# Kernel tuning notes

Hardware: AMD Instinct MI355X
Metric: run time of the kernel (lower is better)

Reference implementation:

```python
import jax, jax.numpy as jnp
import numpy as np

NUM_EMB = 1024
EMB_DIM = 256
COMMITMENT_COST = 0.25


def setup_inputs() -> dict:
    key = jax.random.key(0)
    k1, k2 = jax.random.split(key)
    inp = jax.random.normal(k1, (64, EMB_DIM, 32, 32), dtype=jnp.float32)  # [B, C, H, W]
    emb_weight = jax.random.uniform(
        k2, (NUM_EMB, EMB_DIM), minval=-1.0 / NUM_EMB, maxval=1.0 / NUM_EMB, dtype=jnp.float32
    )
    return {"inp": inp, "emb_weight": emb_weight}


def reference(inp, emb_weight):
    sg = jax.lax.stop_gradient
    x = jnp.transpose(inp, (0, 2, 3, 1))              # [B, H, W, C]
    flat = x.reshape(-1, EMB_DIM)                      # [N, C]
    d = (jnp.sum(flat * flat, axis=1, keepdims=True)
         + jnp.sum(emb_weight * emb_weight, axis=1)
         - 2.0 * (flat @ emb_weight.T))
    idx = jnp.argmin(d, axis=1)                        # [N]
    encodings = jax.nn.one_hot(idx, NUM_EMB, dtype=jnp.float32)  # [N, K]
    e = emb_weight[idx].reshape(x.shape)               # [B, H, W, C]
    loss = jnp.mean((e - sg(x)) ** 2) + COMMITMENT_COST * jnp.mean((sg(e) - x) ** 2)
    e_ste = x + sg(e - x)                              # straight-through estimator
    avg_probs = jnp.mean(encodings, axis=0)
    perplexity = jnp.exp(-jnp.sum(avg_probs * jnp.log(avg_probs + 1e-10)))
    out = jnp.transpose(e_ste, (0, 3, 1, 2))           # back to [B, C, H, W]
    return loss, out, perplexity, encodings
```

## Files before the change

kernel.cpp:

```cpp
#include <hip/hip_runtime.h>
#include <hip/hip_bf16.h>
#include <math.h>
#include <float.h>

#define BB    64
#define CCH   256
#define KKE   1024
#define HWN   1024
#define NTOT  (BB*HWN)
#define OUT_ELE (BB*CCH*HWN)
#define LOSS_OFF 0
#define OUT_OFF  1
#define PERP_OFF (1 + OUT_ELE)
#define ENC_OFF  (2 + OUT_ELE)

#define WS_IDX    0
#define WS_ANORM  262144
#define WS_HIST   524288
#define WS_BNORM  528384
#define WS_MISC   532480
#define WS_LIST   536576
#define WS_EMBT   798720
#define WS_EHI    1847296
#define WS_ELO    2371584
#define WS_CD1    2895872
#define WS_CK1    4993024
#define WS_CD2    7090176

typedef __attribute__((ext_vector_type(4))) float f32x4;
typedef __attribute__((ext_vector_type(8))) short s16x8;

#define TAU 2e-4f

__device__ inline void merge_cand(float& d1, int& k1, float& d2,
                                  float od1, int ok1, float od2) {
    bool w = (od1 < d1) || (od1 == d1 && ok1 < k1);
    float loser_d1 = w ? d1 : od1;
    float winner_d2 = w ? od2 : d2;
    d2 = fminf(winner_d2, loser_d1);
    if (w) { d1 = od1; k1 = ok1; }
}

__global__ __launch_bounds__(256) void prep_kernel(const float* __restrict__ emb,
                                                   float* __restrict__ embT,
                                                   float* __restrict__ bnorm,
                                                   short* __restrict__ ehi,
                                                   short* __restrict__ elo,
                                                   unsigned int* __restrict__ hist,
                                                   float* __restrict__ misc) {
    const int k = blockIdx.x;
    const int t = threadIdx.x;
    float v = emb[k*CCH + t];
    embT[(size_t)t*KKE + k] = v;
    __hip_bfloat16 h = __float2bfloat16(v);
    float hf = __bfloat162float(h);
    __hip_bfloat16 l = __float2bfloat16(v - hf);
    size_t eoff = (size_t)(t >> 5)*32768 + (size_t)k*32 + (t & 31);
    ehi[eoff] = *(short*)&h;
    elo[eoff] = *(short*)&l;
    double sq = (double)v * (double)v;
    #pragma unroll
    for (int off = 32; off; off >>= 1) sq += __shfl_down(sq, off);
    __shared__ double wred[4];
    const int wave = t >> 6, lane = t & 63;
    if (lane == 0) wred[wave] = sq;
    __syncthreads();
    if (t == 0) bnorm[k] = (float)(wred[0] + wred[1] + wred[2] + wred[3]);
    if (blockIdx.x < 4) hist[blockIdx.x*256 + t] = 0u;
    if (blockIdx.x == 4 && t == 0) { misc[0] = 0.0f; ((int*)misc)[1] = 0; }
}

__global__ __launch_bounds__(256) void anorm_kernel(const float* __restrict__ inp,
                                                    float* __restrict__ anorm) {
    const int b  = blockIdx.y;
    const int hw = blockIdx.x * 256 + threadIdx.x;
    const float* p = inp + (size_t)b*CCH*HWN + hw;
    double s = 0.0;
    #pragma unroll 8
    for (int c = 0; c < CCH; ++c) {
        float v = p[(size_t)c*HWN];
        s += (double)v * (double)v;
    }
    anorm[b*HWN + hw] = (float)s;
}

__global__ __launch_bounds__(256, 3) void argmin_mfma(const float* __restrict__ inp,
                                                      const short* __restrict__ ehi,
                                                      const short* __restrict__ elo,
                                                      const float* __restrict__ anorm,
                                                      const float* __restrict__ bnorm,
                                                      float* __restrict__ cd1,
                                                      int* __restrict__ ck1,
                                                      float* __restrict__ cd2) {
    __shared__ short Ahi[128*40];
    __shared__ short Alo[128*40];
    __shared__ short Bhi[128*40];
    __shared__ short Blo[128*40];

    const int t    = threadIdx.x;
    const int w    = t >> 6;
    const int lane = t & 63;
    const int q    = lane >> 4;
    const int l15  = lane & 15;
    const int n0   = blockIdx.x * 128;
    const int k0   = blockIdx.y * 128;
    const int b    = n0 >> 10;
    const int hw0  = n0 & 1023;
    const float* gA = inp + (size_t)b*CCH*HWN + hw0;

    const int na = t & 127;
    const int ch = t >> 7;
    const int br = t >> 2;
    const int bc = (t & 3) * 8;

    f32x4 acc[2][8];
    #pragma unroll
    for (int i = 0; i < 2; ++i)
        #pragma unroll
        for (int j = 0; j < 8; ++j) acc[i][j] = (f32x4){0.f,0.f,0.f,0.f};

    for (int chunk = 0; chunk < 8; ++chunk) {
        const int c0 = chunk * 32;
        __syncthreads();
        float v[16];
        #pragma unroll
        for (int cc = 0; cc < 16; ++cc)
            v[cc] = gA[(size_t)(c0 + ch*16 + cc) * HWN + na];
        short hs[16], ls[16];
        #pragma unroll
        for (int cc = 0; cc < 16; ++cc) {
            __hip_bfloat16 h = __float2bfloat16(v[cc]);
            float hf = __bfloat162float(h);
            __hip_bfloat16 l = __float2bfloat16(v[cc] - hf);
            hs[cc] = *(short*)&h; ls[cc] = *(short*)&l;
        }
        *(s16x8*)&Ahi[na*40 + ch*16]     = *(s16x8*)&hs[0];
        *(s16x8*)&Ahi[na*40 + ch*16 + 8] = *(s16x8*)&hs[8];
        *(s16x8*)&Alo[na*40 + ch*16]     = *(s16x8*)&ls[0];
        *(s16x8*)&Alo[na*40 + ch*16 + 8] = *(s16x8*)&ls[8];
        {
            const size_t ebase = (size_t)chunk*32768 + (size_t)k0*32;
            *(s16x8*)&Bhi[br*40 + bc]        = *(const s16x8*)&ehi[ebase + t*8];
            *(s16x8*)&Bhi[(64+br)*40 + bc]   = *(const s16x8*)&ehi[ebase + 2048 + t*8];
            *(s16x8*)&Blo[br*40 + bc]        = *(const s16x8*)&elo[ebase + t*8];
            *(s16x8*)&Blo[(64+br)*40 + bc]   = *(const s16x8*)&elo[ebase + 2048 + t*8];
        }
        __syncthreads();
        s16x8 afh0 = *(s16x8*)&Ahi[(w*32 +      l15)*40 + q*8];
        s16x8 afh1 = *(s16x8*)&Ahi[(w*32 + 16 + l15)*40 + q*8];
        s16x8 afl0 = *(s16x8*)&Alo[(w*32 +      l15)*40 + q*8];
        s16x8 afl1 = *(s16x8*)&Alo[(w*32 + 16 + l15)*40 + q*8];
        #pragma unroll
        for (int ct = 0; ct < 8; ++ct) {
            s16x8 bh = *(s16x8*)&Bhi[(ct*16 + l15)*40 + q*8];
            s16x8 bl = *(s16x8*)&Blo[(ct*16 + l15)*40 + q*8];
            acc[0][ct] = __builtin_amdgcn_mfma_f32_16x16x32_bf16(afh0, bh, acc[0][ct], 0, 0, 0);
            acc[0][ct] = __builtin_amdgcn_mfma_f32_16x16x32_bf16(afh0, bl, acc[0][ct], 0, 0, 0);
            acc[0][ct] = __builtin_amdgcn_mfma_f32_16x16x32_bf16(afl0, bh, acc[0][ct], 0, 0, 0);
            acc[1][ct] = __builtin_amdgcn_mfma_f32_16x16x32_bf16(afh1, bh, acc[1][ct], 0, 0, 0);
            acc[1][ct] = __builtin_amdgcn_mfma_f32_16x16x32_bf16(afh1, bl, acc[1][ct], 0, 0, 0);
            acc[1][ct] = __builtin_amdgcn_mfma_f32_16x16x32_bf16(afl1, bh, acc[1][ct], 0, 0, 0);
        }
    }

    float bnv[8];
    #pragma unroll
    for (int ct = 0; ct < 8; ++ct) bnv[ct] = bnorm[k0 + ct*16 + l15];

    #pragma unroll
    for (int rg = 0; rg < 2; ++rg) {
        #pragma unroll
        for (int reg = 0; reg < 4; ++reg) {
            const int n = n0 + w*32 + rg*16 + q*4 + reg;
            const float a = anorm[n];
            float d1 = FLT_MAX, d2 = FLT_MAX; int k1 = 0;
            #pragma unroll
            for (int ct = 0; ct < 8; ++ct) {
                float s = a + bnv[ct];
                float d = s - 2.0f * acc[rg][ct][reg];
                int   k = k0 + ct*16 + l15;
                if (d < d1 || (d == d1 && k < k1)) { d2 = d1; d1 = d; k1 = k; }
                else d2 = fminf(d2, d);
            }
            #pragma unroll
            for (int off = 1; off < 16; off <<= 1) {
                float od1 = __shfl_xor(d1, off);
                int   ok1 = __shfl_xor(k1, off);
                float od2 = __shfl_xor(d2, off);
                merge_cand(d1, k1, d2, od1, ok1, od2);
            }
            if (l15 == 0) {
                const size_t o = (size_t)blockIdx.y*NTOT + n;
                cd1[o] = d1; ck1[o] = k1; cd2[o] = d2;
            }
        }
    }
}

__global__ __launch_bounds__(256) void reduce_kernel(const float* __restrict__ cd1,
                                                     const int* __restrict__ ck1,
                                                     const float* __restrict__ cd2,
                                                     int* __restrict__ idx,
                                                     int* __restrict__ list,
                                                     int* __restrict__ counter) {
    const int n = blockIdx.x*256 + threadIdx.x;
    float d1 = cd1[n]; int k1 = ck1[n]; float d2 = cd2[n];
    #pragma unroll
    for (int kb = 1; kb < 8; ++kb) {
        const size_t o = (size_t)kb*NTOT + n;
        merge_cand(d1, k1, d2, cd1[o], ck1[o], cd2[o]);
    }
    idx[n] = k1;
    if (d2 - d1 < TAU) {
        int p = atomicAdd(counter, 1);
        list[p] = n;
    }
}

__global__ __launch_bounds__(256) void rescore_kernel(const float* __restrict__ inp,
                                                      const float* __restrict__ embT,
                                                      const float* __restrict__ anorm,
                                                      const float* __restrict__ bnorm,
                                                      const int* __restrict__ list,
                                                      const int* __restrict__ counter,
                                                      int* __restrict__ idx) {
    __shared__ float xs[256];
    __shared__ float rd[256];
    __shared__ int   rk[256];
    const int t = threadIdx.x;
    const int cnt = *counter;
    for (int f = blockIdx.x; f < cnt; f += gridDim.x) {
        const int n = list[f];
        const int b = n >> 10, hw = n & 1023;
        __syncthreads();
        xs[t] = inp[(size_t)b*CCH*HWN + (size_t)t*HWN + hw];
        __syncthreads();
        float dot0 = 0.f, dot1 = 0.f, dot2 = 0.f, dot3 = 0.f;
        #pragma unroll 4
        for (int c = 0; c < CCH; ++c) {
            const float xc = xs[c];
            const float* row = embT + (size_t)c*KKE + t;
            dot0 += xc * row[0];
            dot1 += xc * row[256];
            dot2 += xc * row[512];
            dot3 += xc * row[768];
        }
        const float a = anorm[n];
        float bd = FLT_MAX; int bk = 0;
        float dots[4] = {dot0, dot1, dot2, dot3};
        #pragma unroll
        for (int kk = 0; kk < 4; ++kk) {
            const int k = kk*256 + t;
            float s = a + bnorm[k];
            float d = s - 2.0f * dots[kk];
            if (d < bd || (d == bd && k < bk)) { bd = d; bk = k; }
        }
        rd[t] = bd; rk[t] = bk;
        __syncthreads();
        for (int stride = 128; stride; stride >>= 1) {
            if (t < stride) {
                float od = rd[t+stride]; int ok = rk[t+stride];
                if (od < rd[t] || (od == rd[t] && ok < rk[t])) { rd[t] = od; rk[t] = ok; }
            }
            __syncthreads();
        }
        if (t == 0) idx[n] = rk[0];
    }
}

__global__ __launch_bounds__(256) void onehot_kernel(const int* __restrict__ idx,
                                                     float* __restrict__ enc,
                                                     unsigned int* __restrict__ hist) {
    const int t = threadIdx.x;
    const int j4 = t * 4;
    for (int r = 0; r < 16; ++r) {
        const int n = blockIdx.x*16 + r;
        const int k = idx[n];
        float2 v0 = {0.0f, 0.0f}, v1 = {0.0f, 0.0f};
        if (k == j4)     v0.x = 1.0f;
        if (k == j4 + 1) v0.y = 1.0f;
        if (k == j4 + 2) v1.x = 1.0f;
        if (k == j4 + 3) v1.y = 1.0f;
        float* row = enc + (size_t)n * KKE;
        *(float2*)&row[j4]     = v0;
        *(float2*)&row[j4 + 2] = v1;
        if (t == 0) atomicAdd(&hist[k], 1u);
    }
}

__global__ __launch_bounds__(256) void out_loss_kernel(const float* __restrict__ inp,
                                                       const float* __restrict__ embT,
                                                       const int* __restrict__ idx,
                                                       float* __restrict__ out,
                                                       float* __restrict__ lossacc) {
    const int t = threadIdx.x;
    const size_t stride = (size_t)gridDim.x * 256;
    float lsum = 0.0f;
    for (size_t m = (size_t)blockIdx.x * 256 + t; m < (size_t)OUT_ELE; m += stride) {
        int hw = (int)(m & 1023);
        int c  = (int)((m >> 10) & 255);
        int b  = (int)(m >> 18);
        int k  = idx[b*HWN + hw];
        float e = embT[(size_t)c*KKE + k];
        float x = inp[m];
        out[m] = e;
        float df = e - x;
        lsum += df * df;
    }
    #pragma unroll
    for (int off = 32; off; off >>= 1) lsum += __shfl_down(lsum, off);
    __shared__ float wred[4];
    const int wave = t >> 6, lane = t & 63;
    if (lane == 0) wred[wave] = lsum;
    __syncthreads();
    if (t == 0) atomicAdd(lossacc, wred[0] + wred[1] + wred[2] + wred[3]);
}

__global__ __launch_bounds__(1024) void final_kernel(const unsigned int* __restrict__ hist,
                                                     const float* __restrict__ lossacc,
                                                     float* __restrict__ d_out) {
    const int t = threadIdx.x;
    float p = (float)hist[t] * (1.0f / 65536.0f);
    float v = p * logf(p + 1e-10f);
    #pragma unroll
    for (int off = 32; off; off >>= 1) v += __shfl_down(v, off);
    __shared__ float wred[16];
    const int wave = t >> 6, lane = t & 63;
    if (lane == 0) wred[wave] = v;
    __syncthreads();
    if (t == 0) {
        float s = 0.0f;
        #pragma unroll
        for (int i = 0; i < 16; ++i) s += wred[i];
        d_out[PERP_OFF] = expf(-s);
        d_out[LOSS_OFF] = 1.25f * (*lossacc) * (1.0f / (float)OUT_ELE);
    }
}

extern "C" void kernel_launch(void* const* d_in, const int* in_sizes, int n_in,
                              void* d_out, int out_size, void* d_ws, size_t ws_size,
                              hipStream_t stream) {
    (void)in_sizes; (void)n_in; (void)out_size; (void)ws_size;
    const float* inp = (const float*)d_in[0];
    const float* emb = (const float*)d_in[1];
    float* out = (float*)d_out;
    char* ws = (char*)d_ws;
    int*          idx     = (int*)(ws + WS_IDX);
    float*        anorm   = (float*)(ws + WS_ANORM);
    unsigned int* hist    = (unsigned int*)(ws + WS_HIST);
    float*        bnorm   = (float*)(ws + WS_BNORM);
    float*        misc    = (float*)(ws + WS_MISC);
    int*          list    = (int*)(ws + WS_LIST);
    float*        embT    = (float*)(ws + WS_EMBT);
    short*        ehi     = (short*)(ws + WS_EHI);
    short*        elo     = (short*)(ws + WS_ELO);
    float*        cd1     = (float*)(ws + WS_CD1);
    int*          ck1     = (int*)(ws + WS_CK1);
    float*        cd2     = (float*)(ws + WS_CD2);
    int*          counter = ((int*)misc) + 1;

    prep_kernel<<<dim3(KKE), dim3(256), 0, stream>>>(emb, embT, bnorm, ehi, elo, hist, misc);
    anorm_kernel<<<dim3(4, BB), dim3(256), 0, stream>>>(inp, anorm);
    argmin_mfma<<<dim3(512, 8), dim3(256), 0, stream>>>(inp, ehi, elo, anorm, bnorm, cd1, ck1, cd2);
    reduce_kernel<<<dim3(256), dim3(256), 0, stream>>>(cd1, ck1, cd2, idx, list, counter);
    rescore_kernel<<<dim3(512), dim3(256), 0, stream>>>(inp, embT, anorm, bnorm, list, counter, idx);
    onehot_kernel<<<dim3(4096), dim3(256), 0, stream>>>(idx, out + ENC_OFF, hist);
    out_loss_kernel<<<dim3(4096), dim3(256), 0, stream>>>(inp, embT, idx, out + OUT_OFF, misc);
    final_kernel<<<dim3(1), dim3(1024), 0, stream>>>(hist, misc, out);
}
```

Measured before the change: 745.2 us.

## Use 2x2 wave tiling in argmin MFMA kernel with LDS cross-wave merge

Reorganizes the four waves of the distance/argmin kernel into a 2x2 grid of 64x64 sub-tiles instead of four 32x128 row strips, reducing per-wave LDS fragment loads for the hi/lo bf16 split products. The per-block top-2 candidates from the two k-halves are merged through shared memory before writing out. The LDS row padding also changes from 40 to 36 shorts, which alters bank mapping and alignment of vector LDS accesses, and adds an extra barrier and shared-memory traffic in the epilogue.

Result: slower. 761.6 us (+2.2%).

```diff
diff --git a/kernel.cpp b/kernel.cpp
--- a/kernel.cpp
+++ b/kernel.cpp
@@ -31,6 +31,7 @@
 typedef __attribute__((ext_vector_type(8))) short s16x8;
 
 #define TAU 2e-4f
+#define APAD 36
 
 __device__ inline void merge_cand(float& d1, int& k1, float& d2,
                                   float od1, int ok1, float od2) {
@@ -92,16 +93,22 @@
                                                       float* __restrict__ cd1,
                                                       int* __restrict__ ck1,
                                                       float* __restrict__ cd2) {
-    __shared__ short Ahi[128*40];
-    __shared__ short Alo[128*40];
-    __shared__ short Bhi[128*40];
-    __shared__ short Blo[128*40];
+    __shared__ short Ahi[128*APAD];
+    __shared__ short Alo[128*APAD];
+    __shared__ short Bhi[128*APAD];
+    __shared__ short Blo[128*APAD];
+    __shared__ float m_d1[2][128];
+    __shared__ float m_d2[2][128];
+    __shared__ int   m_k1[2][128];
 
     const int t    = threadIdx.x;
     const int w    = t >> 6;
     const int lane = t & 63;
     const int q    = lane >> 4;
     const int l15  = lane & 15;
+    const int wn   = (w & 1) * 64;
+    const int wkh  = w >> 1;
+    const int wk   = wkh * 64;
     const int n0   = blockIdx.x * 128;
     const int k0   = blockIdx.y * 128;
     const int b    = n0 >> 10;
@@ -113,11 +120,11 @@
     const int br = t >> 2;
     const int bc = (t & 3) * 8;
 
-    f32x4 acc[2][8];
-    #pragma unroll
-    for (int i = 0; i < 2; ++i)
-        #pragma unroll
-        for (int j = 0; j < 8; ++j) acc[i][j] = (f32x4){0.f,0.f,0.f,0.f};
+    f32x4 acc[4][4];
+    #pragma unroll
+    for (int i = 0; i < 4; ++i)
+        #pragma unroll
+        for (int j = 0; j < 4; ++j) acc[i][j] = (f32x4){0.f,0.f,0.f,0.f};
 
     for (int chunk = 0; chunk < 8; ++chunk) {
         const int c0 = chunk * 32;
@@ -134,51 +141,53 @@
             __hip_bfloat16 l = __float2bfloat16(v[cc] - hf);
             hs[cc] = *(short*)&h; ls[cc] = *(short*)&l;
         }
-        *(s16x8*)&Ahi[na*40 + ch*16]     = *(s16x8*)&hs[0];
-        *(s16x8*)&Ahi[na*40 + ch*16 + 8] = *(s16x8*)&hs[8];
-        *(s16x8*)&Alo[na*40 + ch*16]     = *(s16x8*)&ls[0];
-        *(s16x8*)&Alo[na*40 + ch*16 + 8] = *(s16x8*)&ls[8];
+        *(s16x8*)&Ahi[na*APAD + ch*16]     = *(s16x8*)&hs[0];
+        *(s16x8*)&Ahi[na*APAD + ch*16 + 8] = *(s16x8*)&hs[8];
+        *(s16x8*)&Alo[na*APAD + ch*16]     = *(s16x8*)&ls[0];
+        *(s16x8*)&Alo[na*APAD + ch*16 + 8] = *(s16x8*)&ls[8];
         {
             const size_t ebase = (size_t)chunk*32768 + (size_t)k0*32;
-            *(s16x8*)&Bhi[br*40 + bc]        = *(const s16x8*)&ehi[ebase + t*8];
-            *(s16x8*)&Bhi[(64+br)*40 + bc]   = *(const s16x8*)&ehi[ebase + 2048 + t*8];
-            *(s16x8*)&Blo[br*40 + bc]        = *(const s16x8*)&elo[ebase + t*8];
-            *(s16x8*)&Blo[(64+br)*40 + bc]   = *(const s16x8*)&elo[ebase + 2048 + t*8];
-        }
-        __syncthreads();
-        s16x8 afh0 = *(s16x8*)&Ahi[(w*32 +      l15)*40 + q*8];
-        s16x8 afh1 = *(s16x8*)&Ahi[(w*32 + 16 + l15)*40 + q*8];
-        s16x8 afl0 = *(s16x8*)&Alo[(w*32 +      l15)*40 + q*8];
-        s16x8 afl1 = *(s16x8*)&Alo[(w*32 + 16 + l15)*40 + q*8];
-        #pragma unroll
-        for (int ct = 0; ct < 8; ++ct) {
-            s16x8 bh = *(s16x8*)&Bhi[(ct*16 + l15)*40 + q*8];
-            s16x8 bl = *(s16x8*)&Blo[(ct*16 + l15)*40 + q*8];
-            acc[0][ct] = __builtin_amdgcn_mfma_f32_16x16x32_bf16(afh0, bh, acc[0][ct], 0, 0, 0);
-            acc[0][ct] = __builtin_amdgcn_mfma_f32_16x16x32_bf16(afh0, bl, acc[0][ct], 0, 0, 0);
-            acc[0][ct] = __builtin_amdgcn_mfma_f32_16x16x32_bf16(afl0, bh, acc[0][ct], 0, 0, 0);
-            acc[1][ct] = __builtin_amdgcn_mfma_f32_16x16x32_bf16(afh1, bh, acc[1][ct], 0, 0, 0);
-            acc[1][ct] = __builtin_amdgcn_mfma_f32_16x16x32_bf16(afh1, bl, acc[1][ct], 0, 0, 0);
-            acc[1][ct] = __builtin_amdgcn_mfma_f32_16x16x32_bf16(afl1, bh, acc[1][ct], 0, 0, 0);
-        }
-    }
-
-    float bnv[8];
-    #pragma unroll
-    for (int ct = 0; ct < 8; ++ct) bnv[ct] = bnorm[k0 + ct*16 + l15];
-
-    #pragma unroll
-    for (int rg = 0; rg < 2; ++rg) {
+            *(s16x8*)&Bhi[br*APAD + bc]      = *(const s16x8*)&ehi[ebase + t*8];
+            *(s16x8*)&Bhi[(64+br)*APAD + bc] = *(const s16x8*)&ehi[ebase + 2048 + t*8];
+            *(s16x8*)&Blo[br*APAD + bc]      = *(const s16x8*)&elo[ebase + t*8];
+            *(s16x8*)&Blo[(64+br)*APAD + bc] = *(const s16x8*)&elo[ebase + 2048 + t*8];
+        }
+        __syncthreads();
+        s16x8 ah[4], al[4];
+        #pragma unroll
+        for (int rg = 0; rg < 4; ++rg) {
+            ah[rg] = *(s16x8*)&Ahi[(wn + rg*16 + l15)*APAD + q*8];
+            al[rg] = *(s16x8*)&Alo[(wn + rg*16 + l15)*APAD + q*8];
+        }
+        #pragma unroll
+        for (int ct = 0; ct < 4; ++ct) {
+            s16x8 bh = *(s16x8*)&Bhi[(wk + ct*16 + l15)*APAD + q*8];
+            s16x8 bl = *(s16x8*)&Blo[(wk + ct*16 + l15)*APAD + q*8];
+            #pragma unroll
+            for (int rg = 0; rg < 4; ++rg) {
+                acc[rg][ct] = __builtin_amdgcn_mfma_f32_16x16x32_bf16(ah[rg], bh, acc[rg][ct], 0, 0, 0);
+                acc[rg][ct] = __builtin_amdgcn_mfma_f32_16x16x32_bf16(ah[rg], bl, acc[rg][ct], 0, 0, 0);
+                acc[rg][ct] = __builtin_amdgcn_mfma_f32_16x16x32_bf16(al[rg], bh, acc[rg][ct], 0, 0, 0);
+            }
+        }
+    }
+
+    float bnv[4];
+    #pragma unroll
+    for (int ct = 0; ct < 4; ++ct) bnv[ct] = bnorm[k0 + wk + ct*16 + l15];
+
+    #pragma unroll
+    for (int rg = 0; rg < 4; ++rg) {
         #pragma unroll
         for (int reg = 0; reg < 4; ++reg) {
-            const int n = n0 + w*32 + rg*16 + q*4 + reg;
-            const float a = anorm[n];
+            const int nl = wn + rg*16 + q*4 + reg;
+            const float a = anorm[n0 + nl];
             float d1 = FLT_MAX, d2 = FLT_MAX; int k1 = 0;
             #pragma unroll
-            for (int ct = 0; ct < 8; ++ct) {
+            for (int ct = 0; ct < 4; ++ct) {
                 float s = a + bnv[ct];
                 float d = s - 2.0f * acc[rg][ct][reg];
-                int   k = k0 + ct*16 + l15;
+                int   k = k0 + wk + ct*16 + l15;
                 if (d < d1 || (d == d1 && k < k1)) { d2 = d1; d1 = d; k1 = k; }
                 else d2 = fminf(d2, d);
             }
@@ -190,10 +199,16 @@
                 merge_cand(d1, k1, d2, od1, ok1, od2);
             }
             if (l15 == 0) {
-                const size_t o = (size_t)blockIdx.y*NTOT + n;
-                cd1[o] = d1; ck1[o] = k1; cd2[o] = d2;
-            }
-        }
+                m_d1[wkh][nl] = d1; m_k1[wkh][nl] = k1; m_d2[wkh][nl] = d2;
+            }
+        }
+    }
+    __syncthreads();
+    if (t < 128) {
+        float d1 = m_d1[0][t]; int k1 = m_k1[0][t]; float d2 = m_d2[0][t];
+        merge_cand(d1, k1, d2, m_d1[1][t], m_k1[1][t], m_d2[1][t]);
+        const size_t o = (size_t)blockIdx.y*NTOT + n0 + t;
+        cd1[o] = d1; ck1[o] = k1; cd2[o] = d2;
     }
 }
 
```
